# Optimization experiments

Measured on AMD Instinct MI355X. Metric: run time of the kernel, lower is better.

The kernel has to match this reference:

```python
import jax, jax.numpy as jnp
import numpy as np
import math

L = 16
LOGT = 19
T = 2 ** LOGT
F = 2
NMIN = 16
NMAX = 2048
X_MIN = 0.0
X_MAX = 1.0
N_POINTS = 524288
P1 = np.uint32(2654435761)  # spatial hash prime for y
P2 = np.uint32(805459861)   # spatial hash prime for z


def setup_inputs() -> dict:
    key = jax.random.key(0)
    k1, k2 = jax.random.split(key)
    x = jax.random.uniform(k1, (N_POINTS, 3), dtype=jnp.float32)
    hashmap = jax.random.normal(k2, (L, T, F), dtype=jnp.float32) * 1e-2
    b = math.exp((math.log(NMAX) - math.log(NMIN)) / (L - 1))
    resolution = jnp.asarray(np.floor(NMIN * b ** np.arange(L)), dtype=jnp.float32)
    return {"x": x, "hashmap": hashmap, "resolution": resolution}


def reference(x, hashmap, resolution):
    # normalize coords to [0,1] (x_min=0, x_max=1 here)
    xn = (x - X_MIN) / (X_MAX - X_MIN)
    # per-level scaled coords: [L, n, 3]
    xs = xn[None, :, :] * resolution[:, None, None]
    x0f = jnp.floor(xs)
    w = xs - x0f                                 # trilinear weights [L, n, 3]
    c0 = x0f.astype(jnp.uint32)
    c1 = c0 + jnp.uint32(1)
    hx0, hy0, hz0 = c0[..., 0], c0[..., 1] * P1, c0[..., 2] * P2
    hx1, hy1, hz1 = c1[..., 0], c1[..., 1] * P1, c1[..., 2] * P2
    Tm = jnp.uint32(T - 1)
    # 8 corner hash indices, order 000,001,010,011,100,101,110,111: [L, n, 8]
    idx = jnp.stack([
        (hx0 ^ hy0 ^ hz0) & Tm, (hx0 ^ hy0 ^ hz1) & Tm,
        (hx0 ^ hy1 ^ hz0) & Tm, (hx0 ^ hy1 ^ hz1) & Tm,
        (hx1 ^ hy0 ^ hz0) & Tm, (hx1 ^ hy0 ^ hz1) & Tm,
        (hx1 ^ hy1 ^ hz0) & Tm, (hx1 ^ hy1 ^ hz1) & Tm,
    ], axis=-1).astype(jnp.int32)
    wx, wy, wz = w[..., 0], w[..., 1], w[..., 2]
    wxn, wyn, wzn = 1.0 - wx, 1.0 - wy, 1.0 - wz
    # corner weights matching idx order: [L, n, 8]
    cw = jnp.stack([
        wxn * wyn * wzn, wxn * wyn * wz, wxn * wy * wzn, wxn * wy * wz,
        wx * wyn * wzn, wx * wyn * wz, wx * wy * wzn, wx * wy * wz,
    ], axis=-1)
    # gather per-level corner features: [L, n, 8, F]
    feats = jax.vmap(lambda h, i: h[i])(hashmap, idx)
    # interpolate and lay out as [n, L*F] (level-major, matching kernel store)
    out = jnp.einsum('lnc,lncf->nlf', cw, feats)
    return out.reshape(x.shape[0], L * F)
```

## Files before the change

kernel.cpp:

```cpp
#include <hip/hip_runtime.h>
#include <hip/hip_fp16.h>

namespace {
constexpr unsigned kT  = 1u << 19;
constexpr unsigned kTm = kT - 1u;
constexpr unsigned kP1 = 2654435761u;
constexpr unsigned kP2 = 805459861u;
constexpr int      kNPTS = 524288;

constexpr int      kD[4]        = {17, 23, 31, 43};
constexpr unsigned kCells[4]    = {17u*17u*17u, 23u*23u*23u, 31u*31u*31u, 43u*43u*43u};
constexpr unsigned kCellBase[4] = {0u, 4913u, 17080u, 46871u};
constexpr unsigned kTotCells    = 126378u;
constexpr unsigned kDenseElems  = kTotCells * 8u;
constexpr size_t   kStageOff    = (size_t)4u << 20;
constexpr size_t   kStageBytes  = (size_t)kNPTS * 16u * 8u;
constexpr size_t   kWsNeed      = kStageOff + kStageBytes;

constexpr int kNSeg[8]      = {4,3,3,2,2,3,3,2};
constexpr int kSegLvl[8][4] = {
  {0,1,2,3}, {3,4,5,0}, {5,6,7,0}, {7,8,0,0},
  {9,10,0,0}, {10,11,12,0}, {12,13,14,0}, {14,15,0,0}};
constexpr int kSegBeg[8][4] = {
  {0,0,0,0}, {1024,0,0,0}, {1024,0,0,0}, {512,0,0,0},
  {0,0,0,0}, {1536,0,0,0}, {1024,0,0,0}, {512,0,0,0}};
constexpr int kSegEnd[8][4] = {
  {2048,2048,2048,1024}, {2048,2048,1024,0}, {2048,2048,512,0}, {2048,2048,0,0},
  {2048,1536,0,0}, {2048,2048,1024,0}, {2048,2048,512,0}, {2048,2048,0,0}};
constexpr unsigned kMaxBlk = 7168;
}

typedef float    f32x2 __attribute__((ext_vector_type(2)));
typedef float    f32x4 __attribute__((ext_vector_type(4)));
typedef unsigned u32x4 __attribute__((ext_vector_type(4)));

__device__ inline f32x2 h2_to_f2(unsigned w) {
    __half2 h = __builtin_bit_cast(__half2, w);
    f32x2 r; r.x = __half2float(h.x); r.y = __half2float(h.y);
    return r;
}

__global__ __launch_bounds__(256) void build_dense16(
    const float* __restrict__ hashmap, unsigned* __restrict__ dense16)
{
    unsigned t = blockIdx.x * 256 + threadIdx.x;
    if (t >= kDenseElems) return;
    unsigned cell = t >> 3, corner = t & 7u;
    int l; unsigned rem;
    if      (cell < kCellBase[1]) { l = 0; rem = cell; }
    else if (cell < kCellBase[2]) { l = 1; rem = cell - kCellBase[1]; }
    else if (cell < kCellBase[3]) { l = 2; rem = cell - kCellBase[2]; }
    else                          { l = 3; rem = cell - kCellBase[3]; }
    unsigned D = (unsigned)kD[l];
    unsigned ck = rem % D, tmp = rem / D;
    unsigned cj = tmp % D,  ci = tmp / D;
    unsigned ii = ci + ((corner >> 2) & 1u);
    unsigned jj = cj + ((corner >> 1) & 1u);
    unsigned kk = ck + (corner & 1u);
    unsigned h = (ii ^ (jj * kP1) ^ (kk * kP2)) & kTm;
    f32x2 v = reinterpret_cast<const f32x2*>(hashmap)[(size_t)l * kT + h];
    __half2 p;
    p.x = __float2half_rn(v.x);
    p.y = __float2half_rn(v.y);
    dense16[t] = __builtin_bit_cast(unsigned, p);
}

__global__ __launch_bounds__(256) void hashgrid_gather(
    const float* __restrict__ x,
    const float* __restrict__ hashmap,
    const float* __restrict__ resolution,
    const unsigned* __restrict__ dense16,
    f32x2* __restrict__ stage)
{
    unsigned i = blockIdx.x;
    unsigned g = i & 7u;
    unsigned j = i >> 3;

    int lvl = -1; unsigned chunk = 0, acc = 0;
    #pragma unroll
    for (int s = 0; s < 4; ++s) {
        if (s >= kNSeg[g]) break;
        unsigned len = (unsigned)(kSegEnd[g][s] - kSegBeg[g][s]);
        if (j < acc + len) { lvl = kSegLvl[g][s]; chunk = kSegBeg[g][s] + (j - acc); break; }
        acc += len;
    }
    if (lvl < 0) return;

    int n = (int)(chunk * 256u + threadIdx.x);

    float px = __builtin_nontemporal_load(&x[3*n+0]);
    float py = __builtin_nontemporal_load(&x[3*n+1]);
    float pz = __builtin_nontemporal_load(&x[3*n+2]);
    float res = resolution[lvl];

    float xs = px*res, ys = py*res, zs = pz*res;
    float fx = floorf(xs), fy = floorf(ys), fz = floorf(zs);
    float wx = xs-fx, wy = ys-fy, wz = zs-fz;

    unsigned cx0 = (unsigned)fx;
    unsigned cy0 = (unsigned)fy;
    unsigned cz0 = (unsigned)fz;

    f32x2 f000, f001, f010, f011, f100, f101, f110, f111;

    if (lvl < 4) {
        unsigned D = (unsigned)kD[lvl];
        unsigned cell = (cx0 * D + cy0) * D + cz0;
        const u32x4* blk = reinterpret_cast<const u32x4*>(
            dense16 + ((size_t)kCellBase[lvl] + cell) * 8u);
        u32x4 lo = blk[0], hi = blk[1];
        f000 = h2_to_f2(lo.x); f001 = h2_to_f2(lo.y);
        f010 = h2_to_f2(lo.z); f011 = h2_to_f2(lo.w);
        f100 = h2_to_f2(hi.x); f101 = h2_to_f2(hi.y);
        f110 = h2_to_f2(hi.z); f111 = h2_to_f2(hi.w);
    } else {
        unsigned hy0 = cy0 * kP1, hy1 = (cy0 + 1u) * kP1;
        unsigned hz0 = cz0 * kP2, hz1 = (cz0 + 1u) * kP2;
        unsigned hyz00 = hy0 ^ hz0, hyz01 = hy0 ^ hz1;
        unsigned hyz10 = hy1 ^ hz0, hyz11 = hy1 ^ hz1;
        const f32x2* __restrict__ tb =
            reinterpret_cast<const f32x2*>(hashmap) + (size_t)lvl * kT;

        if ((cx0 & 1u) == 0u) {
            const f32x4* __restrict__ tb4 = reinterpret_cast<const f32x4*>(tb);
            unsigned i00 = (cx0 ^ hyz00) & kTm;
            unsigned i01 = (cx0 ^ hyz01) & kTm;
            unsigned i10 = (cx0 ^ hyz10) & kTm;
            unsigned i11 = (cx0 ^ hyz11) & kTm;
            f32x4 q00 = tb4[i00 >> 1];
            f32x4 q01 = tb4[i01 >> 1];
            f32x4 q10 = tb4[i10 >> 1];
            f32x4 q11 = tb4[i11 >> 1];
            bool o0 = (i00 & 1u), o1 = (i01 & 1u), o2 = (i10 & 1u), o3 = (i11 & 1u);
            f000.x = o0 ? q00.z : q00.x; f000.y = o0 ? q00.w : q00.y;
            f100.x = o0 ? q00.x : q00.z; f100.y = o0 ? q00.y : q00.w;
            f001.x = o1 ? q01.z : q01.x; f001.y = o1 ? q01.w : q01.y;
            f101.x = o1 ? q01.x : q01.z; f101.y = o1 ? q01.y : q01.w;
            f010.x = o2 ? q10.z : q10.x; f010.y = o2 ? q10.w : q10.y;
            f110.x = o2 ? q10.x : q10.z; f110.y = o2 ? q10.y : q10.w;
            f011.x = o3 ? q11.z : q11.x; f011.y = o3 ? q11.w : q11.y;
            f111.x = o3 ? q11.x : q11.z; f111.y = o3 ? q11.y : q11.w;
        } else {
            unsigned hx0 = cx0, hx1 = cx0 + 1u;
            f000 = tb[(hx0 ^ hyz00) & kTm];
            f001 = tb[(hx0 ^ hyz01) & kTm];
            f010 = tb[(hx0 ^ hyz10) & kTm];
            f011 = tb[(hx0 ^ hyz11) & kTm];
            f100 = tb[(hx1 ^ hyz00) & kTm];
            f101 = tb[(hx1 ^ hyz01) & kTm];
            f110 = tb[(hx1 ^ hyz10) & kTm];
            f111 = tb[(hx1 ^ hyz11) & kTm];
        }
    }

    float wxn = 1.f - wx, wyn = 1.f - wy, wzn = 1.f - wz;
    float w000 = wxn*wyn*wzn, w001 = wxn*wyn*wz;
    float w010 = wxn*wy *wzn, w011 = wxn*wy *wz;
    float w100 = wx *wyn*wzn, w101 = wx *wyn*wz;
    float w110 = wx *wy *wzn, w111 = wx *wy *wz;

    f32x2 o;
    o.x = w000*f000.x + w001*f001.x + w010*f010.x + w011*f011.x
        + w100*f100.x + w101*f101.x + w110*f110.x + w111*f111.x;
    o.y = w000*f000.y + w001*f001.y + w010*f010.y + w011*f011.y
        + w100*f100.y + w101*f101.y + w110*f110.y + w111*f111.y;

    __builtin_nontemporal_store(o, &stage[(size_t)lvl * kNPTS + n]);
}

__global__ __launch_bounds__(256) void stage_transpose(
    const f32x2* __restrict__ stage, f32x4* __restrict__ out4)
{
    __shared__ f32x2 tile[128][17];
    unsigned n0 = blockIdx.x * 128u;
    unsigned t = threadIdx.x;

    #pragma unroll
    for (int it = 0; it < 8; ++it) {
        unsigned m = (unsigned)it * 256u + t;
        unsigned l = m >> 7, p = m & 127u;
        tile[p][l] = stage[(size_t)l * kNPTS + n0 + p];
    }
    __syncthreads();

    #pragma unroll
    for (int it = 0; it < 4; ++it) {
        unsigned v = (unsigned)it * 256u + t;
        unsigned p = v >> 3, q = v & 7u;
        f32x2 a = tile[p][2u*q], b = tile[p][2u*q + 1u];
        f32x4 w; w.x = a.x; w.y = a.y; w.z = b.x; w.w = b.y;
        __builtin_nontemporal_store(w, &out4[(size_t)(n0 + p) * 8u + q]);
    }
}

__global__ __launch_bounds__(256) void hashgrid_fwd_lvl(
    const float* __restrict__ x,
    const float* __restrict__ hashmap,
    const float* __restrict__ resolution,
    f32x2* __restrict__ out,
    int npts, unsigned cpl)
{
    unsigned i = blockIdx.x;
    unsigned g = i & 7u;
    unsigned j = i >> 3;
    unsigned phase = j / cpl;
    unsigned chunk = j - phase * cpl;
    unsigned l = g + (phase << 3);

    int n = (int)(chunk * 256u + threadIdx.x);
    if (n >= npts) return;

    float px = x[3*n+0], py = x[3*n+1], pz = x[3*n+2];
    float res = resolution[l];

    float xs = px*res, ys = py*res, zs = pz*res;
    float fx = floorf(xs), fy = floorf(ys), fz = floorf(zs);
    float wx = xs-fx, wy = ys-fy, wz = zs-fz;

    unsigned cx0 = (unsigned)fx, cy0 = (unsigned)fy, cz0 = (unsigned)fz;
    unsigned hx0 = cx0,       hx1 = cx0 + 1u;
    unsigned hy0 = cy0 * kP1, hy1 = (cy0 + 1u) * kP1;
    unsigned hz0 = cz0 * kP2, hz1 = (cz0 + 1u) * kP2;

    const f32x2* __restrict__ tb =
        reinterpret_cast<const f32x2*>(hashmap) + (size_t)l * kT;
    f32x2 f000 = tb[(hx0 ^ hy0 ^ hz0) & kTm];
    f32x2 f001 = tb[(hx0 ^ hy0 ^ hz1) & kTm];
    f32x2 f010 = tb[(hx0 ^ hy1 ^ hz0) & kTm];
    f32x2 f011 = tb[(hx0 ^ hy1 ^ hz1) & kTm];
    f32x2 f100 = tb[(hx1 ^ hy0 ^ hz0) & kTm];
    f32x2 f101 = tb[(hx1 ^ hy0 ^ hz1) & kTm];
    f32x2 f110 = tb[(hx1 ^ hy1 ^ hz0) & kTm];
    f32x2 f111 = tb[(hx1 ^ hy1 ^ hz1) & kTm];

    float wxn = 1.f - wx, wyn = 1.f - wy, wzn = 1.f - wz;
    float w000 = wxn*wyn*wzn, w001 = wxn*wyn*wz;
    float w010 = wxn*wy *wzn, w011 = wxn*wy *wz;
    float w100 = wx *wyn*wzn, w101 = wx *wyn*wz;
    float w110 = wx *wy *wzn, w111 = wx *wy *wz;

    f32x2 o;
    o.x = w000*f000.x + w001*f001.x + w010*f010.x + w011*f011.x
        + w100*f100.x + w101*f101.x + w110*f110.x + w111*f111.x;
    o.y = w000*f000.y + w001*f001.y + w010*f010.y + w011*f011.y
        + w100*f100.y + w101*f101.y + w110*f110.y + w111*f111.y;

    __builtin_nontemporal_store(o, &out[(size_t)n*16 + l]);
}

extern "C" void kernel_launch(void* const* d_in, const int* in_sizes, int n_in,
                              void* d_out, int out_size, void* d_ws, size_t ws_size,
                              hipStream_t stream) {
    const float* x          = (const float*)d_in[0];
    const float* hashmap    = (const float*)d_in[1];
    const float* resolution = (const float*)d_in[2];

    int npts = in_sizes[0] / 3;

    if (npts == kNPTS && d_ws != nullptr && ws_size >= kWsNeed) {
        unsigned* dense16 = (unsigned*)d_ws;
        f32x2* stage = (f32x2*)((char*)d_ws + kStageOff);
        unsigned pb = (kDenseElems + 255u) / 256u;
        build_dense16<<<pb, 256, 0, stream>>>(hashmap, dense16);
        hashgrid_gather<<<8u * kMaxBlk, 256, 0, stream>>>(
            x, hashmap, resolution, dense16, stage);
        stage_transpose<<<kNPTS / 128, 256, 0, stream>>>(
            stage, (f32x4*)d_out);
    } else {
        unsigned cpl = (unsigned)((npts + 255) / 256);
        unsigned blocks = 16u * cpl;
        hashgrid_fwd_lvl<<<blocks, 256, 0, stream>>>(
            x, hashmap, resolution, (f32x2*)d_out, npts, cpl);
    }
}
```

Baseline: 242.8 us.

## Extend dense fp16 corner table to level 4 and rebalance gather block schedule

Adds level 4 (resolution 58) to the prebuilt dense fp16 corner-block table when the workspace is large enough. Dense levels now run in dedicated blocks that each process four 256-point chunks, while hashed levels are redistributed across the eight block groups with a new segment table. The workspace layout is reordered so the stage buffer comes first, and a template parameter picks between the four-level and five-level variants. The intent is to replace eight scattered hash reads with one 32-byte contiguous read for one more level and to balance work per group. The cost is a larger build_dense16 pass (about 2.6M entries instead of about 1M) and fp16 rounding on one more level.

```diff
diff --git a/kernel.cpp b/kernel.cpp
--- a/kernel.cpp
+++ b/kernel.cpp
@@ -8,26 +8,38 @@
 constexpr unsigned kP2 = 805459861u;
 constexpr int      kNPTS = 524288;
 
-constexpr int      kD[4]        = {17, 23, 31, 43};
-constexpr unsigned kCells[4]    = {17u*17u*17u, 23u*23u*23u, 31u*31u*31u, 43u*43u*43u};
-constexpr unsigned kCellBase[4] = {0u, 4913u, 17080u, 46871u};
-constexpr unsigned kTotCells    = 126378u;
-constexpr unsigned kDenseElems  = kTotCells * 8u;
-constexpr size_t   kStageOff    = (size_t)4u << 20;
+constexpr int      kD[5]        = {17, 23, 31, 43, 59};
+constexpr unsigned kCellBase[6] = {0u, 4913u, 17080u, 46871u, 126378u, 331757u};
+constexpr unsigned kDenseElems4 = 126378u * 8u;
+constexpr unsigned kDenseElems5 = 331757u * 8u;
 constexpr size_t   kStageBytes  = (size_t)kNPTS * 16u * 8u;
-constexpr size_t   kWsNeed      = kStageOff + kStageBytes;
-
-constexpr int kNSeg[8]      = {4,3,3,2,2,3,3,2};
-constexpr int kSegLvl[8][4] = {
-  {0,1,2,3}, {3,4,5,0}, {5,6,7,0}, {7,8,0,0},
-  {9,10,0,0}, {10,11,12,0}, {12,13,14,0}, {14,15,0,0}};
-constexpr int kSegBeg[8][4] = {
-  {0,0,0,0}, {1024,0,0,0}, {1024,0,0,0}, {512,0,0,0},
-  {0,0,0,0}, {1536,0,0,0}, {1024,0,0,0}, {512,0,0,0}};
-constexpr int kSegEnd[8][4] = {
-  {2048,2048,2048,1024}, {2048,2048,1024,0}, {2048,2048,512,0}, {2048,2048,0,0},
-  {2048,1536,0,0}, {2048,2048,1024,0}, {2048,2048,512,0}, {2048,2048,0,0}};
-constexpr unsigned kMaxBlk = 7168;
+constexpr size_t   kDenseOff    = kStageBytes;
+constexpr size_t   kWsNeedB     = kDenseOff + (size_t)kDenseElems4 * 4u;
+constexpr size_t   kWsNeedA     = kDenseOff + (size_t)kDenseElems5 * 4u;
+
+constexpr int kDBLK[2]       = {2048, 2560};
+constexpr unsigned kMaxBlkV[2] = {3447, 3283};
+constexpr int kHSeg[2][8][3][3] = {
+ {
+  {{ 4,   0,1399},{-1,0,0},{-1,0,0}},
+  {{ 4,1399,2048},{ 5,0,2048},{ 6,0, 614}},
+  {{ 6, 614,2048},{ 7,0,1877},{-1,0,0}},
+  {{ 7,1877,2048},{ 8,0,2048},{ 9,0,1092}},
+  {{ 9,1092,2048},{10,0,2048},{11,0, 307}},
+  {{11, 307,2048},{12,0,1570},{-1,0,0}},
+  {{12,1570,2048},{13,0,2048},{14,0, 785}},
+  {{14, 785,2048},{15,0,2048},{-1,0,0}},
+ },
+ {
+  {{ 5,   0, 723},{-1,0,0},{-1,0,0}},
+  {{ 5, 723,2048},{ 6,0,1790},{-1,0,0}},
+  {{ 6,1790,2048},{ 7,0,2048},{ 8,0, 809}},
+  {{ 8, 809,2048},{ 9,0,1876},{-1,0,0}},
+  {{ 9,1876,2048},{10,0,2048},{11,0, 895}},
+  {{11, 895,2048},{12,0,1962},{-1,0,0}},
+  {{12,1962,2048},{13,0,2048},{14,0, 981}},
+  {{14, 981,2048},{15,0,2048},{-1,0,0}},
+ }};
 }
 
 typedef float    f32x2 __attribute__((ext_vector_type(2)));
@@ -41,16 +53,18 @@
 }
 
 __global__ __launch_bounds__(256) void build_dense16(
-    const float* __restrict__ hashmap, unsigned* __restrict__ dense16)
+    const float* __restrict__ hashmap, unsigned* __restrict__ dense16,
+    unsigned elems)
 {
     unsigned t = blockIdx.x * 256 + threadIdx.x;
-    if (t >= kDenseElems) return;
+    if (t >= elems) return;
     unsigned cell = t >> 3, corner = t & 7u;
     int l; unsigned rem;
     if      (cell < kCellBase[1]) { l = 0; rem = cell; }
     else if (cell < kCellBase[2]) { l = 1; rem = cell - kCellBase[1]; }
     else if (cell < kCellBase[3]) { l = 2; rem = cell - kCellBase[2]; }
-    else                          { l = 3; rem = cell - kCellBase[3]; }
+    else if (cell < kCellBase[4]) { l = 3; rem = cell - kCellBase[3]; }
+    else                          { l = 4; rem = cell - kCellBase[4]; }
     unsigned D = (unsigned)kD[l];
     unsigned ck = rem % D, tmp = rem / D;
     unsigned cj = tmp % D,  ci = tmp / D;
@@ -65,6 +79,7 @@
     dense16[t] = __builtin_bit_cast(unsigned, p);
 }
 
+template <int V>
 __global__ __launch_bounds__(256) void hashgrid_gather(
     const float* __restrict__ x,
     const float* __restrict__ hashmap,
@@ -75,18 +90,64 @@
     unsigned i = blockIdx.x;
     unsigned g = i & 7u;
     unsigned j = i >> 3;
-
+    unsigned tid = threadIdx.x;
+
+    if (g == 0u && j < (unsigned)kDBLK[V]) {
+        unsigned dc0 = j * 4u;
+        int l = (int)(dc0 >> 11);
+        unsigned c0 = dc0 & 2047u;
+        float res = resolution[l];
+        unsigned D = (unsigned)kD[l];
+        const unsigned* __restrict__ tbl = dense16 + (size_t)kCellBase[l] * 8u;
+
+        #pragma unroll
+        for (int p = 0; p < 4; ++p) {
+            int n = (int)((c0 + (unsigned)p) * 256u + tid);
+            float px = __builtin_nontemporal_load(&x[3*n+0]);
+            float py = __builtin_nontemporal_load(&x[3*n+1]);
+            float pz = __builtin_nontemporal_load(&x[3*n+2]);
+            float xs = px*res, ys = py*res, zs = pz*res;
+            float fx = floorf(xs), fy = floorf(ys), fz = floorf(zs);
+            float wx = xs-fx, wy = ys-fy, wz = zs-fz;
+            unsigned cx0 = (unsigned)fx, cy0 = (unsigned)fy, cz0 = (unsigned)fz;
+            unsigned cell = (cx0 * D + cy0) * D + cz0;
+            const u32x4* blk = reinterpret_cast<const u32x4*>(tbl + (size_t)cell * 8u);
+            u32x4 lo = blk[0], hi = blk[1];
+            f32x2 f000 = h2_to_f2(lo.x), f001 = h2_to_f2(lo.y);
+            f32x2 f010 = h2_to_f2(lo.z), f011 = h2_to_f2(lo.w);
+            f32x2 f100 = h2_to_f2(hi.x), f101 = h2_to_f2(hi.y);
+            f32x2 f110 = h2_to_f2(hi.z), f111 = h2_to_f2(hi.w);
+
+            float wxn = 1.f - wx, wyn = 1.f - wy, wzn = 1.f - wz;
+            float w000 = wxn*wyn*wzn, w001 = wxn*wyn*wz;
+            float w010 = wxn*wy *wzn, w011 = wxn*wy *wz;
+            float w100 = wx *wyn*wzn, w101 = wx *wyn*wz;
+            float w110 = wx *wy *wzn, w111 = wx *wy *wz;
+
+            f32x2 o;
+            o.x = w000*f000.x + w001*f001.x + w010*f010.x + w011*f011.x
+                + w100*f100.x + w101*f101.x + w110*f110.x + w111*f111.x;
+            o.y = w000*f000.y + w001*f001.y + w010*f010.y + w011*f011.y
+                + w100*f100.y + w101*f101.y + w110*f110.y + w111*f111.y;
+            __builtin_nontemporal_store(o, &stage[(size_t)l * kNPTS + n]);
+        }
+        return;
+    }
+
+    unsigned jj = (g == 0u) ? j - (unsigned)kDBLK[V] : j;
     int lvl = -1; unsigned chunk = 0, acc = 0;
     #pragma unroll
-    for (int s = 0; s < 4; ++s) {
-        if (s >= kNSeg[g]) break;
-        unsigned len = (unsigned)(kSegEnd[g][s] - kSegBeg[g][s]);
-        if (j < acc + len) { lvl = kSegLvl[g][s]; chunk = kSegBeg[g][s] + (j - acc); break; }
+    for (int s = 0; s < 3; ++s) {
+        int l0 = kHSeg[V][g][s][0];
+        if (l0 < 0) break;
+        unsigned beg = (unsigned)kHSeg[V][g][s][1];
+        unsigned len = (unsigned)kHSeg[V][g][s][2] - beg;
+        if (jj < acc + len) { lvl = l0; chunk = beg + (jj - acc); break; }
         acc += len;
     }
     if (lvl < 0) return;
 
-    int n = (int)(chunk * 256u + threadIdx.x);
+    int n = (int)(chunk * 256u + tid);
 
     float px = __builtin_nontemporal_load(&x[3*n+0]);
     float py = __builtin_nontemporal_load(&x[3*n+1]);
@@ -97,60 +158,46 @@
     float fx = floorf(xs), fy = floorf(ys), fz = floorf(zs);
     float wx = xs-fx, wy = ys-fy, wz = zs-fz;
 
-    unsigned cx0 = (unsigned)fx;
-    unsigned cy0 = (unsigned)fy;
-    unsigned cz0 = (unsigned)fz;
+    unsigned cx0 = (unsigned)fx, cy0 = (unsigned)fy, cz0 = (unsigned)fz;
 
     f32x2 f000, f001, f010, f011, f100, f101, f110, f111;
 
-    if (lvl < 4) {
-        unsigned D = (unsigned)kD[lvl];
-        unsigned cell = (cx0 * D + cy0) * D + cz0;
-        const u32x4* blk = reinterpret_cast<const u32x4*>(
-            dense16 + ((size_t)kCellBase[lvl] + cell) * 8u);
-        u32x4 lo = blk[0], hi = blk[1];
-        f000 = h2_to_f2(lo.x); f001 = h2_to_f2(lo.y);
-        f010 = h2_to_f2(lo.z); f011 = h2_to_f2(lo.w);
-        f100 = h2_to_f2(hi.x); f101 = h2_to_f2(hi.y);
-        f110 = h2_to_f2(hi.z); f111 = h2_to_f2(hi.w);
+    unsigned hy0 = cy0 * kP1, hy1 = (cy0 + 1u) * kP1;
+    unsigned hz0 = cz0 * kP2, hz1 = (cz0 + 1u) * kP2;
+    unsigned hyz00 = hy0 ^ hz0, hyz01 = hy0 ^ hz1;
+    unsigned hyz10 = hy1 ^ hz0, hyz11 = hy1 ^ hz1;
+    const f32x2* __restrict__ tb =
+        reinterpret_cast<const f32x2*>(hashmap) + (size_t)lvl * kT;
+
+    if ((cx0 & 1u) == 0u) {
+        const f32x4* __restrict__ tb4 = reinterpret_cast<const f32x4*>(tb);
+        unsigned i00 = (cx0 ^ hyz00) & kTm;
+        unsigned i01 = (cx0 ^ hyz01) & kTm;
+        unsigned i10 = (cx0 ^ hyz10) & kTm;
+        unsigned i11 = (cx0 ^ hyz11) & kTm;
+        f32x4 q00 = tb4[i00 >> 1];
+        f32x4 q01 = tb4[i01 >> 1];
+        f32x4 q10 = tb4[i10 >> 1];
+        f32x4 q11 = tb4[i11 >> 1];
+        bool o0 = (i00 & 1u), o1 = (i01 & 1u), o2 = (i10 & 1u), o3 = (i11 & 1u);
+        f000.x = o0 ? q00.z : q00.x; f000.y = o0 ? q00.w : q00.y;
+        f100.x = o0 ? q00.x : q00.z; f100.y = o0 ? q00.y : q00.w;
+        f001.x = o1 ? q01.z : q01.x; f001.y = o1 ? q01.w : q01.y;
+        f101.x = o1 ? q01.x : q01.z; f101.y = o1 ? q01.y : q01.w;
+        f010.x = o2 ? q10.z : q10.x; f010.y = o2 ? q10.w : q10.y;
+        f110.x = o2 ? q10.x : q10.z; f110.y = o2 ? q10.y : q10.w;
+        f011.x = o3 ? q11.z : q11.x; f011.y = o3 ? q11.w : q11.y;
+        f111.x = o3 ? q11.x : q11.z; f111.y = o3 ? q11.y : q11.w;
     } else {
-        unsigned hy0 = cy0 * kP1, hy1 = (cy0 + 1u) * kP1;
-        unsigned hz0 = cz0 * kP2, hz1 = (cz0 + 1u) * kP2;
-        unsigned hyz00 = hy0 ^ hz0, hyz01 = hy0 ^ hz1;
-        unsigned hyz10 = hy1 ^ hz0, hyz11 = hy1 ^ hz1;
-        const f32x2* __restrict__ tb =
-            reinterpret_cast<const f32x2*>(hashmap) + (size_t)lvl * kT;
-
-        if ((cx0 & 1u) == 0u) {
-            const f32x4* __restrict__ tb4 = reinterpret_cast<const f32x4*>(tb);
-            unsigned i00 = (cx0 ^ hyz00) & kTm;
-            unsigned i01 = (cx0 ^ hyz01) & kTm;
-            unsigned i10 = (cx0 ^ hyz10) & kTm;
-            unsigned i11 = (cx0 ^ hyz11) & kTm;
-            f32x4 q00 = tb4[i00 >> 1];
-            f32x4 q01 = tb4[i01 >> 1];
-            f32x4 q10 = tb4[i10 >> 1];
-            f32x4 q11 = tb4[i11 >> 1];
-            bool o0 = (i00 & 1u), o1 = (i01 & 1u), o2 = (i10 & 1u), o3 = (i11 & 1u);
-            f000.x = o0 ? q00.z : q00.x; f000.y = o0 ? q00.w : q00.y;
-            f100.x = o0 ? q00.x : q00.z; f100.y = o0 ? q00.y : q00.w;
-            f001.x = o1 ? q01.z : q01.x; f001.y = o1 ? q01.w : q01.y;
-            f101.x = o1 ? q01.x : q01.z; f101.y = o1 ? q01.y : q01.w;
-            f010.x = o2 ? q10.z : q10.x; f010.y = o2 ? q10.w : q10.y;
-            f110.x = o2 ? q10.x : q10.z; f110.y = o2 ? q10.y : q10.w;
-            f011.x = o3 ? q11.z : q11.x; f011.y = o3 ? q11.w : q11.y;
-            f111.x = o3 ? q11.x : q11.z; f111.y = o3 ? q11.y : q11.w;
-        } else {
-            unsigned hx0 = cx0, hx1 = cx0 + 1u;
-            f000 = tb[(hx0 ^ hyz00) & kTm];
-            f001 = tb[(hx0 ^ hyz01) & kTm];
-            f010 = tb[(hx0 ^ hyz10) & kTm];
-            f011 = tb[(hx0 ^ hyz11) & kTm];
-            f100 = tb[(hx1 ^ hyz00) & kTm];
-            f101 = tb[(hx1 ^ hyz01) & kTm];
-            f110 = tb[(hx1 ^ hyz10) & kTm];
-            f111 = tb[(hx1 ^ hyz11) & kTm];
-        }
+        unsigned hx0 = cx0, hx1 = cx0 + 1u;
+        f000 = tb[(hx0 ^ hyz00) & kTm];
+        f001 = tb[(hx0 ^ hyz01) & kTm];
+        f010 = tb[(hx0 ^ hyz10) & kTm];
+        f011 = tb[(hx0 ^ hyz11) & kTm];
+        f100 = tb[(hx1 ^ hyz00) & kTm];
+        f101 = tb[(hx1 ^ hyz01) & kTm];
+        f110 = tb[(hx1 ^ hyz10) & kTm];
+        f111 = tb[(hx1 ^ hyz11) & kTm];
     }
 
     float wxn = 1.f - wx, wyn = 1.f - wy, wzn = 1.f - wz;
@@ -257,13 +304,20 @@
 
     int npts = in_sizes[0] / 3;
 
-    if (npts == kNPTS && d_ws != nullptr && ws_size >= kWsNeed) {
-        unsigned* dense16 = (unsigned*)d_ws;
-        f32x2* stage = (f32x2*)((char*)d_ws + kStageOff);
-        unsigned pb = (kDenseElems + 255u) / 256u;
-        build_dense16<<<pb, 256, 0, stream>>>(hashmap, dense16);
-        hashgrid_gather<<<8u * kMaxBlk, 256, 0, stream>>>(
-            x, hashmap, resolution, dense16, stage);
+    if (npts == kNPTS && d_ws != nullptr && ws_size >= kWsNeedB) {
+        bool a = (ws_size >= kWsNeedA);
+        f32x2*    stage   = (f32x2*)d_ws;
+        unsigned* dense16 = (unsigned*)((char*)d_ws + kDenseOff);
+        unsigned elems = a ? kDenseElems5 : kDenseElems4;
+        build_dense16<<<(elems + 255u) / 256u, 256, 0, stream>>>(
+            hashmap, dense16, elems);
+        if (a) {
+            hashgrid_gather<1><<<8u * kMaxBlkV[1], 256, 0, stream>>>(
+                x, hashmap, resolution, dense16, stage);
+        } else {
+            hashgrid_gather<0><<<8u * kMaxBlkV[0], 256, 0, stream>>>(
+                x, hashmap, resolution, dense16, stage);
+        }
         stage_transpose<<<kNPTS / 128, 256, 0, stream>>>(
             stage, (f32x4*)d_out);
     } else {
```

Measured after the change: 261.0 us. 7.5% more time.
